# Kernel optimization log

Measured on AMD Instinct MI355X. Metric: run time of the kernel, lower is better.

Reference implementation:

```python
import jax, jax.numpy as jnp
import numpy as np

EPS = 1e-8

def _qparams(x, bits):
    # AsymmetricSignedQParams + GlobalMinMaxObserver: per-tensor min/max,
    # signed range [-2^(b-1), 2^(b-1)-1], asymmetric zero point.
    qmin = -(2 ** (bits - 1))
    qmax = 2 ** (bits - 1) - 1
    mn = jnp.minimum(jnp.min(x), 0.0)
    mx = jnp.maximum(jnp.max(x), 0.0)
    scale = jnp.maximum((mx - mn) / (qmax - qmin), EPS)
    zp = jnp.clip(jnp.round(qmin - mn / scale), qmin, qmax)
    return scale, zp, qmin, qmax

def _fake_quant(x, bits):
    # quantize -> clamp -> dequantize (simulated fixed-point as in float forward)
    scale, zp, qmin, qmax = _qparams(x, bits)
    q = jnp.clip(jnp.round(x / scale) + zp, qmin, qmax)
    return (q - zp) * scale


def setup_inputs() -> dict:
    key = jax.random.key(0)
    k1, k2, k3 = jax.random.split(key, 3)
    B, W, H, D = 8, 1024, 8, 64
    q = jax.random.normal(k1, (B, W, H, D), dtype=jnp.float32)
    k = jax.random.normal(k2, (B, W, H, D), dtype=jnp.float32)
    v = jax.random.normal(k3, (B, W, H, D), dtype=jnp.float32)
    return {"q": q, "k": k, "v": v, "quant_bits": 8}


def reference(q, k, v, quant_bits):
    bits = int(quant_bits)
    d_model = q.shape[-1]
    inv_sqrt_d = 1.0 / np.sqrt(d_model)

    # quantize-dequantize inputs (inputs_{q,k,v}_QParams)
    qf = _fake_quant(q, bits)
    kf = _fake_quant(k, bits)
    vf = _fake_quant(v, bits)

    # matrix_multi_score: quantized QK^T with folded 1/sqrt(d) scale,
    # then requantize output (matrix_multi_score.outputs_QParams)
    scores = jnp.einsum("bqhd,bkhd->bhqk", qf, kf) * inv_sqrt_d
    scores = _fake_quant(scores, bits)

    # SoftmaxLUT: softmax over last dim, result requantized (softmax.outputs_QParams)
    att = jax.nn.softmax(scores, axis=-1)
    att_q = _fake_quant(att, bits)

    # matrix_multi_att: quantized att @ V, requantized output
    context = jnp.einsum("bhqk,bkhd->bqhd", att_q, vf)
    context = _fake_quant(context, bits)

    return context, att_q
```

## Files before the change

kernel.cpp:

```cpp
#include <hip/hip_runtime.h>
#include <cstdint>
#include <cstddef>

#define W  1024
#define NH 8
#define NB 8
#define DH 64
#define BHN (NB*NH)
#define CTX_ELEMS ((size_t)NB*W*NH*DH)
#define NS 64
#define ROWF 512
#define L2E 1.4426950408889634f

typedef int v4i __attribute__((ext_vector_type(4)));


__device__ __forceinline__ unsigned enc_f(float f){
  unsigned u = __float_as_uint(f);
  return (u & 0x80000000u) ? ~u : (u | 0x80000000u);
}
__device__ __forceinline__ float dec_f(unsigned k){
  unsigned u = (k & 0x80000000u) ? (k ^ 0x80000000u) : ~k;
  return __uint_as_float(u);
}

__device__ __forceinline__ float fq1(float x, float s, float z, float mn, float mx){
  float t = rintf(x / s) + z;
  t = fminf(fmaxf(t, mn), mx);
  return (t - z) * s;
}
__device__ __forceinline__ int qint_m(float x, float is, float z, float mn, float mx){
  return (int)fminf(fmaxf(rintf(x * is) + z, mn), mx);
}
__device__ __forceinline__ unsigned pack4(int a0, int a1, int a2, int a3){
  return (unsigned)(a0 & 0xff) | ((unsigned)(a1 & 0xff) << 8) |
         ((unsigned)(a2 & 0xff) << 16) | ((unsigned)(a3 & 0xff) << 24);
}

__device__ __forceinline__ unsigned* slot_min(unsigned* s, int t){ return s + (size_t)(2*t)*NS; }
__device__ __forceinline__ unsigned* slot_max(unsigned* s, int t){ return s + (size_t)(2*t+1)*NS; }

struct QP { float s, z; };

__device__ __forceinline__ QP qp_generic(const unsigned* slots, int t, float qmn, float qmx){
  const unsigned* pm = slots + (size_t)(2*t)*NS;
  const unsigned* px = pm + NS;
  unsigned em = pm[0], ex = px[0];
  for (int i = 1; i < NS; ++i){
    unsigned a = pm[i], b = px[i];
    em = (a < em) ? a : em;
    ex = (b > ex) ? b : ex;
  }
  float mn = dec_f(em), mx = dec_f(ex);
  QP r;
  r.s = fmaxf((mx - mn) / (qmx - qmn), 1e-8f);
  r.z = fminf(fmaxf(rintf(qmn - mn / r.s), qmn), qmx);
  return r;
}
__device__ __forceinline__ QP qp_scores(const int* jmn, const int* jmx, float sq, float sk,
                                        float qmn, float qmx){
  int em = jmn[0], ex = jmx[0];
  for (int i = 1; i < NS; ++i){ em = min(em, jmn[i]); ex = max(ex, jmx[i]); }
  float cfac = 0.125f * (sq * sk);
  float mn = fminf(cfac * (float)em, 0.0f);
  float mx = fmaxf(cfac * (float)ex, 0.0f);
  QP r;
  r.s = fmaxf((mx - mn) / (qmx - qmn), 1e-8f);
  r.z = fminf(fmaxf(rintf(qmn - mn / r.s), qmn), qmx);
  return r;
}

__device__ __forceinline__ void blk_minmax_atomic(float lmin, float lmax,
                                                  unsigned* smin, unsigned* smax){
  #pragma unroll
  for (int o = 32; o; o >>= 1){
    lmin = fminf(lmin, __shfl_xor(lmin, o));
    lmax = fmaxf(lmax, __shfl_xor(lmax, o));
  }
  __shared__ float wmn[4], wmx[4];
  int wid = threadIdx.x >> 6, lane = threadIdx.x & 63;
  if (lane == 0){ wmn[wid] = lmin; wmx[wid] = lmax; }
  __syncthreads();
  if (threadIdx.x == 0){
    float a = wmn[0], b = wmx[0];
    for (int w = 1; w < (int)(blockDim.x >> 6); ++w){
      a = fminf(a, wmn[w]); b = fmaxf(b, wmx[w]);
    }
    atomicMin(smin, enc_f(a));
    atomicMax(smax, enc_f(b));
  }
}

__device__ __forceinline__ void blk_iminmax_atomic(int lmin, int lmax, int* gmin, int* gmax){
  #pragma unroll
  for (int o = 32; o; o >>= 1){
    lmin = min(lmin, __shfl_xor(lmin, o));
    lmax = max(lmax, __shfl_xor(lmax, o));
  }
  __shared__ int iwmn[4], iwmx[4];
  int wid = threadIdx.x >> 6, lane = threadIdx.x & 63;
  if (lane == 0){ iwmn[wid] = lmin; iwmx[wid] = lmax; }
  __syncthreads();
  if (threadIdx.x == 0){
    int a = iwmn[0], b = iwmx[0];
    for (int w = 1; w < (int)(blockDim.x >> 6); ++w){
      a = min(a, iwmn[w]); b = max(b, iwmx[w]);
    }
    atomicMin(gmin, a);
    atomicMax(gmax, b);
  }
}

__device__ __forceinline__ void stage_tile(const float* __restrict__ rowptr,
                                           signed char (*S)[80], int* __restrict__ Ssum,
                                           float is, float z, float mn, float mx, int t){
  const int rr = t >> 2, dq = (t & 3) << 4;
  const float* p = rowptr + (size_t)rr * ROWF + dq;
  int part = 0;
  #pragma unroll
  for (int g = 0; g < 4; ++g){
    float4 x = *(const float4*)(p + g * 4);
    int a0 = qint_m(x.x, is, z, mn, mx), a1 = qint_m(x.y, is, z, mn, mx);
    int a2 = qint_m(x.z, is, z, mn, mx), a3 = qint_m(x.w, is, z, mn, mx);
    part += a0 + a1 + a2 + a3;
    *(unsigned*)&S[rr][dq + g*4] = pack4(a0, a1, a2, a3);
  }
  int x1 = part + __shfl_xor(part, 1);
  int tot = x1 + __shfl_xor(x1, 2);
  if ((t & 3) == 0) Ssum[rr] = tot;
}

__device__ __forceinline__ v4i qfrag_direct(const float* __restrict__ qrow, int lg,
                                            float is, float z, float mn, float mx,
                                            int* sqi_out){
  const float* p = qrow + (lg << 4);
  int part = 0; unsigned d4[4];
  #pragma unroll
  for (int g = 0; g < 4; ++g){
    float4 x = *(const float4*)(p + g * 4);
    int a0 = qint_m(x.x, is, z, mn, mx), a1 = qint_m(x.y, is, z, mn, mx);
    int a2 = qint_m(x.z, is, z, mn, mx), a3 = qint_m(x.w, is, z, mn, mx);
    part += a0 + a1 + a2 + a3;
    d4[g] = pack4(a0, a1, a2, a3);
  }
  part += __shfl_xor(part, 16);
  part += __shfl_xor(part, 32);
  *sqi_out = part;
  v4i r; r[0] = (int)d4[0]; r[1] = (int)d4[1]; r[2] = (int)d4[2]; r[3] = (int)d4[3];
  return r;
}


__global__ void init_slots_kernel(unsigned* __restrict__ slots, int* __restrict__ jmn,
                                  int* __restrict__ jmx, int* __restrict__ Sv8){
  for (int i = threadIdx.x; i < 6*2*NS; i += blockDim.x)
    slots[i] = 0x80000000u;
  if (threadIdx.x < NS){
    jmn[threadIdx.x] = 0x7fffffff;
    jmx[threadIdx.x] = (int)0x80000000;
  }
  for (int i = threadIdx.x; i < BHN*64; i += blockDim.x) Sv8[i] = 0;
}

__global__ __launch_bounds__(256) void minmax3_kernel(const float* __restrict__ q,
                                                      const float* __restrict__ k,
                                                      const float* __restrict__ v,
                                                      unsigned* __restrict__ slots){
  const float4* p = (const float4*)(blockIdx.y == 0 ? q : (blockIdx.y == 1 ? k : v));
  float lmin = 0.f, lmax = 0.f;
  const int n4 = (int)(CTX_ELEMS / 4);
  for (int i = blockIdx.x * blockDim.x + threadIdx.x; i < n4; i += gridDim.x * blockDim.x){
    float4 x = p[i];
    lmin = fminf(lmin, fminf(fminf(x.x, x.y), fminf(x.z, x.w)));
    lmax = fmaxf(lmax, fmaxf(fmaxf(x.x, x.y), fmaxf(x.z, x.w)));
  }
  const int idx = blockIdx.x & (NS - 1);
  blk_minmax_atomic(lmin, lmax, slot_min(slots, blockIdx.y) + idx, slot_max(slots, blockIdx.y) + idx);
}


__global__ __launch_bounds__(256) void pass1a_kernel(const float* __restrict__ kg,
                                                     const float* __restrict__ vg,
                                                     const unsigned* __restrict__ slots,
                                                     const int* __restrict__ bits_p,
                                                     char* __restrict__ k8,
                                                     int* __restrict__ Sk8,
                                                     char* __restrict__ v8,
                                                     int* __restrict__ Sv8){
  __shared__ int ColS[64];
  const int bits = *bits_p;
  const float qmx = (float)((1 << (bits-1)) - 1), qmn = -(float)(1 << (bits-1));
  const QP kp = qp_generic(slots, 1, qmn, qmx);
  const QP vp = qp_generic(slots, 2, qmn, qmx);
  const int it = blockIdx.x, bh = blockIdx.y, b = bh >> 3, h = bh & 7;
  const int i0 = it << 6, t = threadIdx.x;

  {
    const int rr = t >> 2, dq = (t & 3) << 4;
    const float* p = kg + ((size_t)(b*W + i0 + rr) * NH + h) * DH + dq;
    const float isk = 1.0f / kp.s;
    int part = 0; unsigned d4[4];
    #pragma unroll
    for (int g = 0; g < 4; ++g){
      float4 x = *(const float4*)(p + g * 4);
      int a0 = qint_m(x.x, isk, kp.z, qmn, qmx), a1 = qint_m(x.y, isk, kp.z, qmn, qmx);
      int a2 = qint_m(x.z, isk, kp.z, qmn, qmx), a3 = qint_m(x.w, isk, kp.z, qmn, qmx);
      part += a0 + a1 + a2 + a3;
      d4[g] = pack4(a0, a1, a2, a3);
    }
    uint4 u; u.x = d4[0]; u.y = d4[1]; u.z = d4[2]; u.w = d4[3];
    *(uint4*)(k8 + ((size_t)bh << 16) + (((size_t)(i0 + rr)) << 6) + dq) = u;
    int x1 = part + __shfl_xor(part, 1);
    int tot = x1 + __shfl_xor(x1, 2);
    if ((t & 3) == 0) Sk8[(bh << 10) + i0 + rr] = tot;
  }

  {
    const int dq4 = (t & 15) << 2, kb = (t >> 4) << 2;
    const float* vp_ = vg + ((size_t)(b*W + i0 + kb) * NH + h) * DH + dq4;
    const float isv = 1.0f / vp.s;
    float4 x0 = *(const float4*)(vp_);
    float4 x1 = *(const float4*)(vp_ + ROWF);
    float4 x2 = *(const float4*)(vp_ + 2 * ROWF);
    float4 x3 = *(const float4*)(vp_ + 3 * ROWF);
    int q00 = qint_m(x0.x, isv, vp.z, qmn, qmx), q01 = qint_m(x0.y, isv, vp.z, qmn, qmx),
        q02 = qint_m(x0.z, isv, vp.z, qmn, qmx), q03 = qint_m(x0.w, isv, vp.z, qmn, qmx);
    int q10 = qint_m(x1.x, isv, vp.z, qmn, qmx), q11 = qint_m(x1.y, isv, vp.z, qmn, qmx),
        q12 = qint_m(x1.z, isv, vp.z, qmn, qmx), q13 = qint_m(x1.w, isv, vp.z, qmn, qmx);
    int q20 = qint_m(x2.x, isv, vp.z, qmn, qmx), q21 = qint_m(x2.y, isv, vp.z, qmn, qmx),
        q22 = qint_m(x2.z, isv, vp.z, qmn, qmx), q23 = qint_m(x2.w, isv, vp.z, qmn, qmx);
    int q30 = qint_m(x3.x, isv, vp.z, qmn, qmx), q31 = qint_m(x3.y, isv, vp.z, qmn, qmx),
        q32 = qint_m(x3.z, isv, vp.z, qmn, qmx), q33 = qint_m(x3.w, isv, vp.z, qmn, qmx);
    unsigned w0 = pack4(q00, q10, q20, q30);
    unsigned w1 = pack4(q01, q11, q21, q31);
    unsigned w2 = pack4(q02, q12, q22, q32);
    unsigned w3 = pack4(q03, q13, q23, q33);
    char* vb = v8 + ((size_t)bh << 16) + i0 + kb;
    *(unsigned*)(vb + ((size_t)(dq4 + 0) << 10)) = w0;
    *(unsigned*)(vb + ((size_t)(dq4 + 1) << 10)) = w1;
    *(unsigned*)(vb + ((size_t)(dq4 + 2) << 10)) = w2;
    *(unsigned*)(vb + ((size_t)(dq4 + 3) << 10)) = w3;
    int cv0 = q00 + q10 + q20 + q30;
    int cv1 = q01 + q11 + q21 + q31;
    int cv2 = q02 + q12 + q22 + q32;
    int cv3 = q03 + q13 + q23 + q33;
    if (t < 64) ColS[t] = 0;
    __syncthreads();
    atomicAdd(&ColS[dq4 + 0], cv0);
    atomicAdd(&ColS[dq4 + 1], cv1);
    atomicAdd(&ColS[dq4 + 2], cv2);
    atomicAdd(&ColS[dq4 + 3], cv3);
    __syncthreads();
    if (t < 64) atomicAdd(&Sv8[(bh << 6) + t], ColS[t]);
  }
}

__global__ __launch_bounds__(256) void pass1b_kernel(const float* __restrict__ qg,
                                                     const unsigned* __restrict__ slots,
                                                     const int* __restrict__ bits_p,
                                                     float* __restrict__ stash,
                                                     int* __restrict__ jmn,
                                                     int* __restrict__ jmx,
                                                     const char* __restrict__ k8,
                                                     const int* __restrict__ Sk8){
  const int bits = *bits_p;
  const float qmx = (float)((1 << (bits-1)) - 1), qmn = -(float)(1 << (bits-1));
  const QP qq = qp_generic(slots, 0, qmn, qmx);
  const QP kp = qp_generic(slots, 1, qmn, qmx);
  const int it = blockIdx.x, bh = blockIdx.y, b = bh >> 3, h = bh & 7;
  const int i0 = it << 6, t = threadIdx.x;
  const int lane = t & 63, w = t >> 6, lr = lane & 15, lg = lane >> 4;
  const int irow = (w << 4) + lr;
  const int izq = (int)qq.z, izk = (int)kp.z, c64 = 64 * izq * izk;

  int sqi;
  v4i Bq = qfrag_direct(qg + ((size_t)(b*W + i0 + irow) * NH + h) * DH, lg,
                        1.0f / qq.s, qq.z, qmn, qmx, &sqi);
  const char* kb = k8 + ((size_t)bh << 16);
  const int* skb = Sk8 + (bh << 10);

  int gmin = 0x7fffffff, gmax = (int)0x80000000, rmax = (int)0x80000000;
  for (int cc = 0; cc < 16; ++cc){
    #pragma unroll
    for (int jt = 0; jt < 4; ++jt){
      v4i Ak = *(const v4i*)(kb + (((size_t)((cc << 6) + (jt << 4) + lr)) << 6) + (lg << 4));
      v4i s4 = *(const v4i*)(skb + (cc << 6) + (jt << 4) + (lg << 2));
      v4i zz = {0, 0, 0, 0};
      v4i acc = __builtin_amdgcn_mfma_i32_16x16x64_i8(Ak, Bq, zz, 0, 0, 0);
      #pragma unroll
      for (int r = 0; r < 4; ++r){
        int J = acc[r] - izq * s4[r] - izk * sqi + c64;
        gmin = min(gmin, J); gmax = max(gmax, J); rmax = max(rmax, J);
      }
    }
  }
  rmax = max(rmax, __shfl_xor(rmax, 16));
  rmax = max(rmax, __shfl_xor(rmax, 32));
  if (lg == 0)
    stash[((size_t)(b*W + i0 + irow) * NH + h) * DH] = __int_as_float(rmax);
  const int idx = (it + bh * 16) & (NS - 1);
  blk_iminmax_atomic(gmin, gmax, jmn + idx, jmx + idx);
}

__global__ __launch_bounds__(256) void pass2c_kernel(const float* __restrict__ qg,
                                                     unsigned* __restrict__ slots,
                                                     const int* __restrict__ jmn,
                                                     const int* __restrict__ jmx,
                                                     const int* __restrict__ bits_p,
                                                     float* __restrict__ stash,
                                                     const char* __restrict__ k8,
                                                     const int* __restrict__ Sk8){
  const int bits = *bits_p;
  const float qmx = (float)((1 << (bits-1)) - 1), qmn = -(float)(1 << (bits-1));
  const QP qq = qp_generic(slots, 0, qmn, qmx);
  const QP kp = qp_generic(slots, 1, qmn, qmx);
  const QP sp = qp_scores(jmn, jmx, qq.s, kp.s, qmn, qmx);
  const int it = blockIdx.x, bh = blockIdx.y, b = bh >> 3, h = bh & 7;
  const int i0 = it << 6, t = threadIdx.x;
  const int lane = t & 63, w = t >> 6, lr = lane & 15, lg = lane >> 4;
  const int irow = (w << 4) + lr;
  const int izq = (int)qq.z, izk = (int)kp.z, c64 = 64 * izq * izk;
  const float rf = (0.125f * (qq.s * kp.s)) / sp.s;
  const float c2 = sp.s * L2E, zs = sp.z;

  int sqi;
  v4i Bq = qfrag_direct(qg + ((size_t)(b*W + i0 + irow) * NH + h) * DH, lg,
                        1.0f / qq.s, qq.z, qmn, qmx, &sqi);
  int Jm = __float_as_int(stash[((size_t)(b*W + i0 + irow) * NH + h) * DH]);
  const float tmxf = fminf(fmaxf(rintf((float)Jm * rf) + zs, qmn), qmx);
  const char* kb = k8 + ((size_t)bh << 16);
  const int* skb = Sk8 + (bh << 10);

  float zacc = 0.f;
  for (int cc = 0; cc < 16; ++cc){
    #pragma unroll
    for (int jt = 0; jt < 4; ++jt){
      v4i Ak = *(const v4i*)(kb + (((size_t)((cc << 6) + (jt << 4) + lr)) << 6) + (lg << 4));
      v4i s4 = *(const v4i*)(skb + (cc << 6) + (jt << 4) + (lg << 2));
      v4i zz = {0, 0, 0, 0};
      v4i acc = __builtin_amdgcn_mfma_i32_16x16x64_i8(Ak, Bq, zz, 0, 0, 0);
      int J0 = acc[0] - izq * s4[0] - izk * sqi + c64;
      int J1 = acc[1] - izq * s4[1] - izk * sqi + c64;
      int J2 = acc[2] - izq * s4[2] - izk * sqi + c64;
      int J3 = acc[3] - izq * s4[3] - izk * sqi + c64;
      float tl0 = fminf(fmaxf(rintf((float)J0 * rf) + zs, qmn), qmx);
      float tl1 = fminf(fmaxf(rintf((float)J1 * rf) + zs, qmn), qmx);
      float tl2 = fminf(fmaxf(rintf((float)J2 * rf) + zs, qmn), qmx);
      float tl3 = fminf(fmaxf(rintf((float)J3 * rf) + zs, qmn), qmx);
      zacc += exp2f((tl0 - tmxf) * c2);
      zacc += exp2f((tl1 - tmxf) * c2);
      zacc += exp2f((tl2 - tmxf) * c2);
      zacc += exp2f((tl3 - tmxf) * c2);
    }
  }
  zacc += __shfl_xor(zacc, 16);
  zacc += __shfl_xor(zacc, 32);
  if (lg == 0)
    stash[((size_t)(b*W + i0 + irow) * NH + h) * DH + 1] = zacc;
  float ratt = 1.0f / zacc;
  #pragma unroll
  for (int o = 1; o < 16; o <<= 1) ratt = fmaxf(ratt, __shfl_xor(ratt, o));
  if (lane == 0){
    const int idx = ((it << 2) + w + bh * 64) & (NS - 1);
    atomicMax(slot_max(slots, 4) + idx, enc_f(ratt));
  }
}

__global__ __launch_bounds__(256) void pass3c_kernel(const float* __restrict__ qg,
                                                     float* __restrict__ att,
                                                     float* __restrict__ ctx,
                                                     unsigned* __restrict__ slots,
                                                     const int* __restrict__ jmn,
                                                     const int* __restrict__ jmx,
                                                     const int* __restrict__ bits_p,
                                                     const char* __restrict__ k8,
                                                     const int* __restrict__ Sk8,
                                                     const char* __restrict__ v8,
                                                     const int* __restrict__ Sv8){
  __shared__ __align__(16) signed char As[64][80];
  __shared__ int RowA[64];
  const int bits = *bits_p;
  const float qmx = (float)((1 << (bits-1)) - 1), qmn = -(float)(1 << (bits-1));
  const QP qq = qp_generic(slots, 0, qmn, qmx);
  const QP kp = qp_generic(slots, 1, qmn, qmx);
  const QP sp = qp_scores(jmn, jmx, qq.s, kp.s, qmn, qmx);
  const QP vp = qp_generic(slots, 2, qmn, qmx);
  const QP ap = qp_generic(slots, 4, qmn, qmx);
  const int it = blockIdx.x, bh = blockIdx.y, b = bh >> 3, h = bh & 7;
  const int i0 = it << 6, t = threadIdx.x;
  const int lane = t & 63, w = t >> 6, lr = lane & 15, lg = lane >> 4;
  const int irow = (w << 4) + lr;
  const int izq = (int)qq.z, izk = (int)kp.z, c64 = 64 * izq * izk;
  const int iza = (int)ap.z, izv = (int)vp.z;
  const float rf = (0.125f * (qq.s * kp.s)) / sp.s;
  const float c2 = sp.s * L2E, zs = sp.z;
  const float sa = ap.s, za = ap.z, inv_sa = 1.0f / sa;

  int sqi;
  v4i Bq = qfrag_direct(qg + ((size_t)(b*W + i0 + irow) * NH + h) * DH, lg,
                        1.0f / qq.s, qq.z, qmn, qmx, &sqi);
  const size_t rbase = ((size_t)(b*W + i0 + irow) * NH + h) * DH;
  int Jm = __float_as_int(ctx[rbase]);
  const float tmxf = fminf(fmaxf(rintf((float)Jm * rf) + zs, qmn), qmx);
  const float iZ = 1.0f / ctx[rbase + 1];
  const char* kb = k8 + ((size_t)bh << 16);
  const int* skb = Sk8 + (bh << 10);
  const char* vb = v8 + ((size_t)bh << 16);

  int rA = 0;
  v4i accPV[4];
  #pragma unroll
  for (int tj = 0; tj < 4; ++tj){ v4i zz = {0,0,0,0}; accPV[tj] = zz; }

  for (int cc = 0; cc < 16; ++cc){
    #pragma unroll
    for (int jt = 0; jt < 4; ++jt){
      v4i Ak = *(const v4i*)(kb + (((size_t)((cc << 6) + (jt << 4) + lr)) << 6) + (lg << 4));
      v4i s4 = *(const v4i*)(skb + (cc << 6) + (jt << 4) + (lg << 2));
      v4i zz = {0, 0, 0, 0};
      v4i acc = __builtin_amdgcn_mfma_i32_16x16x64_i8(Ak, Bq, zz, 0, 0, 0);
      int J0 = acc[0] - izq * s4[0] - izk * sqi + c64;
      int J1 = acc[1] - izq * s4[1] - izk * sqi + c64;
      int J2 = acc[2] - izq * s4[2] - izk * sqi + c64;
      int J3 = acc[3] - izq * s4[3] - izk * sqi + c64;
      float tl0 = fminf(fmaxf(rintf((float)J0 * rf) + zs, qmn), qmx);
      float tl1 = fminf(fmaxf(rintf((float)J1 * rf) + zs, qmn), qmx);
      float tl2 = fminf(fmaxf(rintf((float)J2 * rf) + zs, qmn), qmx);
      float tl3 = fminf(fmaxf(rintf((float)J3 * rf) + zs, qmn), qmx);
      float p0 = exp2f((tl0 - tmxf) * c2) * iZ;
      float p1 = exp2f((tl1 - tmxf) * c2) * iZ;
      float p2 = exp2f((tl2 - tmxf) * c2) * iZ;
      float p3 = exp2f((tl3 - tmxf) * c2) * iZ;
      float a0 = fminf(fmaxf(rintf(p0 * inv_sa) + za, qmn), qmx);
      float a1 = fminf(fmaxf(rintf(p1 * inv_sa) + za, qmn), qmx);
      float a2 = fminf(fmaxf(rintf(p2 * inv_sa) + za, qmn), qmx);
      float a3 = fminf(fmaxf(rintf(p3 * inv_sa) + za, qmn), qmx);
      float4 y;
      y.x = (a0 - za) * sa; y.y = (a1 - za) * sa;
      y.z = (a2 - za) * sa; y.w = (a3 - za) * sa;
      *(float4*)(att + ((size_t)bh << 20) + (size_t)(i0 + irow) * W
                 + (cc << 6) + (jt << 4) + (lg << 2)) = y;
      int q0 = (int)a0, q1 = (int)a1, q2 = (int)a2, q3 = (int)a3;
      rA += q0 + q1 + q2 + q3;
      *(unsigned*)&As[irow][(jt << 4) + (lg << 2)] = pack4(q0, q1, q2, q3);
    }
    {
      v4i A2 = *(const v4i*)&As[(w << 4) + lr][lg << 4];
      #pragma unroll
      for (int tj = 0; tj < 4; ++tj){
        v4i B2 = *(const v4i*)(vb + (((size_t)((tj << 4) + lr)) << 10) + (cc << 6) + (lg << 4));
        accPV[tj] = __builtin_amdgcn_mfma_i32_16x16x64_i8(A2, B2, accPV[tj], 0, 0, 0);
      }
    }
  }

  rA += __shfl_xor(rA, 16);
  rA += __shfl_xor(rA, 32);
  if (lg == 0) RowA[irow] = rA;

  const float sav = sa * vp.s;
  float lmin = 0.f, lmax = 0.f;
  #pragma unroll
  for (int tj = 0; tj < 4; ++tj){
    const int d = (tj << 4) + lr;
    const int cvd = Sv8[(bh << 6) + d];
    #pragma unroll
    for (int r = 0; r < 4; ++r){
      const int i = (w << 4) + (lg << 2) + r;
      int Jv = accPV[tj][r] - iza * cvd - izv * RowA[i] + 1024 * iza * izv;
      float c = sav * (float)Jv;
      lmin = fminf(lmin, c); lmax = fmaxf(lmax, c);
      ctx[(((size_t)(b * W + i0 + i)) * NH + h) * DH + d] = c;
    }
  }
  const int idx = (it + bh * 16) & (NS - 1);
  blk_minmax_atomic(lmin, lmax, slot_min(slots, 5) + idx, slot_max(slots, 5) + idx);
}


__global__ __launch_bounds__(256) void pass1_plain(const float* __restrict__ qg,
                                                   const float* __restrict__ kg,
                                                   const unsigned* __restrict__ slots,
                                                   const int* __restrict__ bits_p,
                                                   float* __restrict__ stash,
                                                   int* __restrict__ jmn,
                                                   int* __restrict__ jmx){
  __shared__ __align__(16) signed char Qs[64][80], Ks[64][80];
  __shared__ int Sq[64], Sk[64];
  const int bits = *bits_p;
  const float qmx = (float)((1 << (bits-1)) - 1), qmn = -(float)(1 << (bits-1));
  const QP qq = qp_generic(slots, 0, qmn, qmx);
  const QP kp = qp_generic(slots, 1, qmn, qmx);
  const int it = blockIdx.x, bh = blockIdx.y, b = bh >> 3, h = bh & 7;
  const int i0 = it << 6, t = threadIdx.x;
  const int lane = t & 63, w = t >> 6, lr = lane & 15, lg = lane >> 4;
  const float isq = 1.0f / qq.s, isk = 1.0f / kp.s;
  const int izq = (int)qq.z, izk = (int)kp.z, c64 = 64 * izq * izk;

  stage_tile(qg + ((size_t)(b*W + i0) * NH + h) * DH, Qs, Sq, isq, qq.z, qmn, qmx, t);
  __syncthreads();
  const v4i Bq = *(const v4i*)&Qs[(w << 4) + lr][lg << 4];
  const int sqi = Sq[(w << 4) + lr];

  int gmin = 0x7fffffff, gmax = (int)0x80000000, rmax = (int)0x80000000;
  for (int cc = 0; cc < 16; ++cc){
    __syncthreads();
    stage_tile(kg + ((size_t)(b*W + (cc << 6)) * NH + h) * DH, Ks, Sk, isk, kp.z, qmn, qmx, t);
    __syncthreads();
    #pragma unroll
    for (int jt = 0; jt < 4; ++jt){
      v4i Ak = *(const v4i*)&Ks[(jt << 4) + lr][lg << 4];
      v4i zz = {0, 0, 0, 0};
      v4i acc = __builtin_amdgcn_mfma_i32_16x16x64_i8(Ak, Bq, zz, 0, 0, 0);
      v4i s4 = *(const v4i*)&Sk[(jt << 4) + (lg << 2)];
      #pragma unroll
      for (int r = 0; r < 4; ++r){
        int J = acc[r] - izq * s4[r] - izk * sqi + c64;
        gmin = min(gmin, J); gmax = max(gmax, J); rmax = max(rmax, J);
      }
    }
  }
  rmax = max(rmax, __shfl_xor(rmax, 16));
  rmax = max(rmax, __shfl_xor(rmax, 32));
  if (lg == 0)
    stash[((size_t)(b*W + i0 + (w << 4) + lr) * NH + h) * DH] = __int_as_float(rmax);
  const int idx = (it + bh * 16) & (NS - 1);
  blk_iminmax_atomic(gmin, gmax, jmn + idx, jmx + idx);
}

__global__ __launch_bounds__(256) void pass2_plain(const float* __restrict__ qg,
                                                   const float* __restrict__ kg,
                                                   unsigned* __restrict__ slots,
                                                   const int* __restrict__ jmn,
                                                   const int* __restrict__ jmx,
                                                   const int* __restrict__ bits_p,
                                                   float* __restrict__ stash){
  __shared__ __align__(16) signed char Qs[64][80], Ks[64][80];
  __shared__ int Sq[64], Sk[64];
  const int bits = *bits_p;
  const float qmx = (float)((1 << (bits-1)) - 1), qmn = -(float)(1 << (bits-1));
  const QP qq = qp_generic(slots, 0, qmn, qmx);
  const QP kp = qp_generic(slots, 1, qmn, qmx);
  const QP sp = qp_scores(jmn, jmx, qq.s, kp.s, qmn, qmx);
  const int it = blockIdx.x, bh = blockIdx.y, b = bh >> 3, h = bh & 7;
  const int i0 = it << 6, t = threadIdx.x;
  const int lane = t & 63, w = t >> 6, lr = lane & 15, lg = lane >> 4;
  const float isq = 1.0f / qq.s, isk = 1.0f / kp.s;
  const int izq = (int)qq.z, izk = (int)kp.z, c64 = 64 * izq * izk;
  const float rf = (0.125f * (qq.s * kp.s)) / sp.s;
  const float c2 = sp.s * L2E, zs = sp.z;
  const int irow = (w << 4) + lr;

  stage_tile(qg + ((size_t)(b*W + i0) * NH + h) * DH, Qs, Sq, isq, qq.z, qmn, qmx, t);
  __syncthreads();
  const v4i Bq = *(const v4i*)&Qs[irow][lg << 4];
  const int sqi = Sq[irow];
  int Jm = __float_as_int(stash[((size_t)(b*W + i0 + irow) * NH + h) * DH]);
  const float tmxf = fminf(fmaxf(rintf((float)Jm * rf) + zs, qmn), qmx);

  float zacc = 0.f;
  for (int cc = 0; cc < 16; ++cc){
    __syncthreads();
    stage_tile(kg + ((size_t)(b*W + (cc << 6)) * NH + h) * DH, Ks, Sk, isk, kp.z, qmn, qmx, t);
    __syncthreads();
    #pragma unroll
    for (int jt = 0; jt < 4; ++jt){
      v4i Ak = *(const v4i*)&Ks[(jt << 4) + lr][lg << 4];
      v4i zz = {0, 0, 0, 0};
      v4i acc = __builtin_amdgcn_mfma_i32_16x16x64_i8(Ak, Bq, zz, 0, 0, 0);
      v4i s4 = *(const v4i*)&Sk[(jt << 4) + (lg << 2)];
      int J0 = acc[0] - izq * s4[0] - izk * sqi + c64;
      int J1 = acc[1] - izq * s4[1] - izk * sqi + c64;
      int J2 = acc[2] - izq * s4[2] - izk * sqi + c64;
      int J3 = acc[3] - izq * s4[3] - izk * sqi + c64;
      float tl0 = fminf(fmaxf(rintf((float)J0 * rf) + zs, qmn), qmx);
      float tl1 = fminf(fmaxf(rintf((float)J1 * rf) + zs, qmn), qmx);
      float tl2 = fminf(fmaxf(rintf((float)J2 * rf) + zs, qmn), qmx);
      float tl3 = fminf(fmaxf(rintf((float)J3 * rf) + zs, qmn), qmx);
      zacc += exp2f((tl0 - tmxf) * c2);
      zacc += exp2f((tl1 - tmxf) * c2);
      zacc += exp2f((tl2 - tmxf) * c2);
      zacc += exp2f((tl3 - tmxf) * c2);
    }
  }
  zacc += __shfl_xor(zacc, 16);
  zacc += __shfl_xor(zacc, 32);
  if (lg == 0)
    stash[((size_t)(b*W + i0 + irow) * NH + h) * DH + 1] = zacc;
  float ratt = 1.0f / zacc;
  #pragma unroll
  for (int o = 1; o < 16; o <<= 1) ratt = fmaxf(ratt, __shfl_xor(ratt, o));
  if (lane == 0){
    const int idx = ((it << 2) + w + bh * 64) & (NS - 1);
    atomicMax(slot_max(slots, 4) + idx, enc_f(ratt));
  }
}

__global__ __launch_bounds__(256) void pass3_plain(const float* __restrict__ qg,
                                                   const float* __restrict__ kg,
                                                   const float* __restrict__ vg,
                                                   float* __restrict__ att,
                                                   float* __restrict__ ctx,
                                                   unsigned* __restrict__ slots,
                                                   const int* __restrict__ jmn,
                                                   const int* __restrict__ jmx,
                                                   const int* __restrict__ bits_p){
  __shared__ __align__(16) signed char Qs[64][80], Ks[64][80], Vs[64][80], As[64][80];
  __shared__ int Sq[64], Sk[64];
  __shared__ int RowA[64], ColV[64];
  const int bits = *bits_p;
  const float qmx = (float)((1 << (bits-1)) - 1), qmn = -(float)(1 << (bits-1));
  const QP qq = qp_generic(slots, 0, qmn, qmx);
  const QP kp = qp_generic(slots, 1, qmn, qmx);
  const QP sp = qp_scores(jmn, jmx, qq.s, kp.s, qmn, qmx);
  const QP vp = qp_generic(slots, 2, qmn, qmx);
  const QP ap = qp_generic(slots, 4, qmn, qmx);
  const int it = blockIdx.x, bh = blockIdx.y, b = bh >> 3, h = bh & 7;
  const int i0 = it << 6, t = threadIdx.x;
  const int lane = t & 63, w = t >> 6, lr = lane & 15, lg = lane >> 4;
  const float isq = 1.0f / qq.s, isk = 1.0f / kp.s;
  const int izq = (int)qq.z, izk = (int)kp.z, c64 = 64 * izq * izk;
  const float rf = (0.125f * (qq.s * kp.s)) / sp.s;
  const float c2 = sp.s * L2E, zs = sp.z;
  const float sa = ap.s, za = ap.z, inv_sa = 1.0f / sa;
  const float sv = vp.s, zv = vp.z, isv = 1.0f / sv;
  const int iza = (int)za, izv = (int)zv;
  const int irow = (w << 4) + lr;

  if (t < 64) ColV[t] = 0;
  stage_tile(qg + ((size_t)(b*W + i0) * NH + h) * DH, Qs, Sq, isq, qq.z, qmn, qmx, t);
  __syncthreads();
  const v4i Bq = *(const v4i*)&Qs[irow][lg << 4];
  const int sqi = Sq[irow];
  const size_t rbase = ((size_t)(b*W + i0 + irow) * NH + h) * DH;
  int Jm = __float_as_int(ctx[rbase]);
  const float tmxf = fminf(fmaxf(rintf((float)Jm * rf) + zs, qmn), qmx);
  const float iZ = 1.0f / ctx[rbase + 1];

  const int dq4 = (t & 15) << 2;
  const int kb  = (t >> 4) << 2;
  int cv4[4] = {0, 0, 0, 0};
  int rA = 0;
  v4i accPV[4];
  #pragma unroll
  for (int tj = 0; tj < 4; ++tj){ v4i zz = {0,0,0,0}; accPV[tj] = zz; }

  for (int cc = 0; cc < 16; ++cc){
    __syncthreads();
    stage_tile(kg + ((size_t)(b*W + (cc << 6)) * NH + h) * DH, Ks, Sk, isk, kp.z, qmn, qmx, t);
    {
      const float* vp_ = vg + ((size_t)(b*W + (cc << 6) + kb) * NH + h) * DH + dq4;
      float4 x0 = *(const float4*)(vp_);
      float4 x1 = *(const float4*)(vp_ + ROWF);
      float4 x2 = *(const float4*)(vp_ + 2 * ROWF);
      float4 x3 = *(const float4*)(vp_ + 3 * ROWF);
      int q00 = qint_m(x0.x, isv, zv, qmn, qmx), q01 = qint_m(x0.y, isv, zv, qmn, qmx),
          q02 = qint_m(x0.z, isv, zv, qmn, qmx), q03 = qint_m(x0.w, isv, zv, qmn, qmx);
      int q10 = qint_m(x1.x, isv, zv, qmn, qmx), q11 = qint_m(x1.y, isv, zv, qmn, qmx),
          q12 = qint_m(x1.z, isv, zv, qmn, qmx), q13 = qint_m(x1.w, isv, zv, qmn, qmx);
      int q20 = qint_m(x2.x, isv, zv, qmn, qmx), q21 = qint_m(x2.y, isv, zv, qmn, qmx),
          q22 = qint_m(x2.z, isv, zv, qmn, qmx), q23 = qint_m(x2.w, isv, zv, qmn, qmx);
      int q30 = qint_m(x3.x, isv, zv, qmn, qmx), q31 = qint_m(x3.y, isv, zv, qmn, qmx),
          q32 = qint_m(x3.z, isv, zv, qmn, qmx), q33 = qint_m(x3.w, isv, zv, qmn, qmx);
      cv4[0] += q00 + q10 + q20 + q30;
      cv4[1] += q01 + q11 + q21 + q31;
      cv4[2] += q02 + q12 + q22 + q32;
      cv4[3] += q03 + q13 + q23 + q33;
      *(unsigned*)&Vs[dq4 + 0][kb] = pack4(q00, q10, q20, q30);
      *(unsigned*)&Vs[dq4 + 1][kb] = pack4(q01, q11, q21, q31);
      *(unsigned*)&Vs[dq4 + 2][kb] = pack4(q02, q12, q22, q32);
      *(unsigned*)&Vs[dq4 + 3][kb] = pack4(q03, q13, q23, q33);
    }
    __syncthreads();
    #pragma unroll
    for (int jt = 0; jt < 4; ++jt){
      v4i Ak = *(const v4i*)&Ks[(jt << 4) + lr][lg << 4];
      v4i zz = {0, 0, 0, 0};
      v4i acc = __builtin_amdgcn_mfma_i32_16x16x64_i8(Ak, Bq, zz, 0, 0, 0);
      v4i s4 = *(const v4i*)&Sk[(jt << 4) + (lg << 2)];
      int J0 = acc[0] - izq * s4[0] - izk * sqi + c64;
      int J1 = acc[1] - izq * s4[1] - izk * sqi + c64;
      int J2 = acc[2] - izq * s4[2] - izk * sqi + c64;
      int J3 = acc[3] - izq * s4[3] - izk * sqi + c64;
      float tl0 = fminf(fmaxf(rintf((float)J0 * rf) + zs, qmn), qmx);
      float tl1 = fminf(fmaxf(rintf((float)J1 * rf) + zs, qmn), qmx);
      float tl2 = fminf(fmaxf(rintf((float)J2 * rf) + zs, qmn), qmx);
      float tl3 = fminf(fmaxf(rintf((float)J3 * rf) + zs, qmn), qmx);
      float p0 = exp2f((tl0 - tmxf) * c2) * iZ;
      float p1 = exp2f((tl1 - tmxf) * c2) * iZ;
      float p2 = exp2f((tl2 - tmxf) * c2) * iZ;
      float p3 = exp2f((tl3 - tmxf) * c2) * iZ;
      float a0 = fminf(fmaxf(rintf(p0 * inv_sa) + za, qmn), qmx);
      float a1 = fminf(fmaxf(rintf(p1 * inv_sa) + za, qmn), qmx);
      float a2 = fminf(fmaxf(rintf(p2 * inv_sa) + za, qmn), qmx);
      float a3 = fminf(fmaxf(rintf(p3 * inv_sa) + za, qmn), qmx);
      float4 y;
      y.x = (a0 - za) * sa; y.y = (a1 - za) * sa;
      y.z = (a2 - za) * sa; y.w = (a3 - za) * sa;
      *(float4*)(att + ((size_t)bh << 20) + (size_t)(i0 + irow) * W
                 + (cc << 6) + (jt << 4) + (lg << 2)) = y;
      int q0 = (int)a0, q1 = (int)a1, q2 = (int)a2, q3 = (int)a3;
      rA += q0 + q1 + q2 + q3;
      *(unsigned*)&As[irow][(jt << 4) + (lg << 2)] = pack4(q0, q1, q2, q3);
    }
    {
      v4i A2 = *(const v4i*)&As[(w << 4) + lr][lg << 4];
      #pragma unroll
      for (int tj = 0; tj < 4; ++tj){
        v4i B2 = *(const v4i*)&Vs[(tj << 4) + lr][lg << 4];
        accPV[tj] = __builtin_amdgcn_mfma_i32_16x16x64_i8(A2, B2, accPV[tj], 0, 0, 0);
      }
    }
  }

  rA += __shfl_xor(rA, 16);
  rA += __shfl_xor(rA, 32);
  if (lg == 0) RowA[irow] = rA;
  #pragma unroll
  for (int j = 0; j < 4; ++j) atomicAdd(&ColV[dq4 + j], cv4[j]);
  __syncthreads();

  const float sav = sa * sv;
  float lmin = 0.f, lmax = 0.f;
  #pragma unroll
  for (int tj = 0; tj < 4; ++tj){
    const int d = (tj << 4) + lr;
    #pragma unroll
    for (int r = 0; r < 4; ++r){
      const int i = (w << 4) + (lg << 2) + r;
      int Jv = accPV[tj][r] - iza * ColV[d] - izv * RowA[i] + 1024 * iza * izv;
      float c = sav * (float)Jv;
      lmin = fminf(lmin, c); lmax = fmaxf(lmax, c);
      ctx[(((size_t)(b * W + i0 + i)) * NH + h) * DH + d] = c;
    }
  }
  const int idx = (it + bh * 16) & (NS - 1);
  blk_minmax_atomic(lmin, lmax, slot_min(slots, 5) + idx, slot_max(slots, 5) + idx);
}

__global__ __launch_bounds__(256) void quantctx_kernel(float* __restrict__ ctx,
                                                       const unsigned* __restrict__ slots,
                                                       const int* __restrict__ bits_p){
  const int bits = *bits_p;
  const float qmx = (float)((1 << (bits-1)) - 1), qmn = -(float)(1 << (bits-1));
  const QP cp = qp_generic(slots, 5, qmn, qmx);
  size_t i = (size_t)blockIdx.x * blockDim.x + threadIdx.x;
  float4* p = (float4*)ctx;
  float4 x = p[i];
  x.x = fq1(x.x, cp.s, cp.z, qmn, qmx);
  x.y = fq1(x.y, cp.s, cp.z, qmn, qmx);
  x.z = fq1(x.z, cp.s, cp.z, qmn, qmx);
  x.w = fq1(x.w, cp.s, cp.z, qmn, qmx);
  p[i] = x;
}


extern "C" void kernel_launch(void* const* d_in, const int* in_sizes, int n_in,
                              void* d_out, int out_size, void* d_ws, size_t ws_size,
                              hipStream_t stream){
  const float* q = (const float*)d_in[0];
  const float* k = (const float*)d_in[1];
  const float* v = (const float*)d_in[2];
  const int* bits = (const int*)d_in[3];
  float* ctx = (float*)d_out;
  float* att = (float*)d_out + CTX_ELEMS;
  unsigned* slots = (unsigned*)d_ws;
  int* jmn = (int*)((char*)d_ws + 3072);
  int* jmx = (int*)((char*)d_ws + 3328);
  int* Sv8 = (int*)((char*)d_ws + 4096);
  int* Sk8 = (int*)((char*)d_ws + 20480);
  char* k8 = (char*)d_ws + 282624;
  char* v8 = (char*)d_ws + 4476928;
  const bool cached = ws_size >= (size_t)8671232;

  hipLaunchKernelGGL(init_slots_kernel, dim3(1), dim3(256), 0, stream, slots, jmn, jmx, Sv8);
  hipLaunchKernelGGL(minmax3_kernel, dim3(512, 3), dim3(256), 0, stream, q, k, v, slots);
  if (cached){
    hipLaunchKernelGGL(pass1a_kernel, dim3(16, BHN), dim3(256), 0, stream,
                       k, v, slots, bits, k8, Sk8, v8, Sv8);
    hipLaunchKernelGGL(pass1b_kernel, dim3(16, BHN), dim3(256), 0, stream,
                       q, slots, bits, ctx, jmn, jmx, k8, Sk8);
    hipLaunchKernelGGL(pass2c_kernel, dim3(16, BHN), dim3(256), 0, stream,
                       q, slots, jmn, jmx, bits, ctx, k8, Sk8);
    hipLaunchKernelGGL(pass3c_kernel, dim3(16, BHN), dim3(256), 0, stream,
                       q, att, ctx, slots, jmn, jmx, bits, k8, Sk8, v8, Sv8);
  } else {
    hipLaunchKernelGGL(pass1_plain, dim3(16, BHN), dim3(256), 0, stream,
                       q, k, slots, bits, ctx, jmn, jmx);
    hipLaunchKernelGGL(pass2_plain, dim3(16, BHN), dim3(256), 0, stream,
                       q, k, slots, jmn, jmx, bits, ctx);
    hipLaunchKernelGGL(pass3_plain, dim3(16, BHN), dim3(256), 0, stream,
                       q, k, v, att, ctx, slots, jmn, jmx, bits);
  }
  hipLaunchKernelGGL(quantctx_kernel, dim3(4096), dim3(256), 0, stream, ctx, slots, bits);
}
```

Measured before the change: 210.5 us.

## Cache int8-quantized Q once and reuse across passes; nontemporal att stores

Adds a workspace tier that quantizes Q to int8 with row sums once in pass1a, so pass1b, pass2c and pass3c load packed int8 fragments instead of re-reading and re-quantizing fp32 Q three times. The V fragments for the PV MFMA are now loaded at the top of each chunk loop so their latency can overlap with the QK and softmax work. The attention output is written with nontemporal stores to avoid polluting cache. The Q-cache path only runs when the workspace is large enough, and it adds extra writes in pass1a.

```diff
diff --git a/kernel.cpp b/kernel.cpp
--- a/kernel.cpp
+++ b/kernel.cpp
@@ -13,6 +13,7 @@
 #define L2E 1.4426950408889634f
 
 typedef int v4i __attribute__((ext_vector_type(4)));
+typedef float v4f __attribute__((ext_vector_type(4)));
 
 
 __device__ __forceinline__ unsigned enc_f(float f){
@@ -178,15 +179,18 @@
   blk_minmax_atomic(lmin, lmax, slot_min(slots, blockIdx.y) + idx, slot_max(slots, blockIdx.y) + idx);
 }
 
-
-__global__ __launch_bounds__(256) void pass1a_kernel(const float* __restrict__ kg,
+template<bool QC>
+__global__ __launch_bounds__(256) void pass1a_kernel(const float* __restrict__ qg,
+                                                     const float* __restrict__ kg,
                                                      const float* __restrict__ vg,
                                                      const unsigned* __restrict__ slots,
                                                      const int* __restrict__ bits_p,
                                                      char* __restrict__ k8,
                                                      int* __restrict__ Sk8,
                                                      char* __restrict__ v8,
-                                                     int* __restrict__ Sv8){
+                                                     int* __restrict__ Sv8,
+                                                     char* __restrict__ q8,
+                                                     int* __restrict__ Sq8){
   __shared__ int ColS[64];
   const int bits = *bits_p;
   const float qmx = (float)((1 << (bits-1)) - 1), qmn = -(float)(1 << (bits-1));
@@ -194,9 +198,9 @@
   const QP vp = qp_generic(slots, 2, qmn, qmx);
   const int it = blockIdx.x, bh = blockIdx.y, b = bh >> 3, h = bh & 7;
   const int i0 = it << 6, t = threadIdx.x;
+  const int rr = t >> 2, dq = (t & 3) << 4;
 
   {
-    const int rr = t >> 2, dq = (t & 3) << 4;
     const float* p = kg + ((size_t)(b*W + i0 + rr) * NH + h) * DH + dq;
     const float isk = 1.0f / kp.s;
     int part = 0; unsigned d4[4];
@@ -214,7 +218,25 @@
     int tot = x1 + __shfl_xor(x1, 2);
     if ((t & 3) == 0) Sk8[(bh << 10) + i0 + rr] = tot;
   }
-
+  if (QC){
+    const QP qq = qp_generic(slots, 0, qmn, qmx);
+    const float* p = qg + ((size_t)(b*W + i0 + rr) * NH + h) * DH + dq;
+    const float isq = 1.0f / qq.s;
+    int part = 0; unsigned d4[4];
+    #pragma unroll
+    for (int g = 0; g < 4; ++g){
+      float4 x = *(const float4*)(p + g * 4);
+      int a0 = qint_m(x.x, isq, qq.z, qmn, qmx), a1 = qint_m(x.y, isq, qq.z, qmn, qmx);
+      int a2 = qint_m(x.z, isq, qq.z, qmn, qmx), a3 = qint_m(x.w, isq, qq.z, qmn, qmx);
+      part += a0 + a1 + a2 + a3;
+      d4[g] = pack4(a0, a1, a2, a3);
+    }
+    uint4 u; u.x = d4[0]; u.y = d4[1]; u.z = d4[2]; u.w = d4[3];
+    *(uint4*)(q8 + ((size_t)bh << 16) + (((size_t)(i0 + rr)) << 6) + dq) = u;
+    int x1 = part + __shfl_xor(part, 1);
+    int tot = x1 + __shfl_xor(x1, 2);
+    if ((t & 3) == 0) Sq8[(bh << 10) + i0 + rr] = tot;
+  }
   {
     const int dq4 = (t & 15) << 2, kb = (t >> 4) << 2;
     const float* vp_ = vg + ((size_t)(b*W + i0 + kb) * NH + h) * DH + dq4;
@@ -231,30 +253,38 @@
         q22 = qint_m(x2.z, isv, vp.z, qmn, qmx), q23 = qint_m(x2.w, isv, vp.z, qmn, qmx);
     int q30 = qint_m(x3.x, isv, vp.z, qmn, qmx), q31 = qint_m(x3.y, isv, vp.z, qmn, qmx),
         q32 = qint_m(x3.z, isv, vp.z, qmn, qmx), q33 = qint_m(x3.w, isv, vp.z, qmn, qmx);
-    unsigned w0 = pack4(q00, q10, q20, q30);
-    unsigned w1 = pack4(q01, q11, q21, q31);
-    unsigned w2 = pack4(q02, q12, q22, q32);
-    unsigned w3 = pack4(q03, q13, q23, q33);
     char* vb = v8 + ((size_t)bh << 16) + i0 + kb;
-    *(unsigned*)(vb + ((size_t)(dq4 + 0) << 10)) = w0;
-    *(unsigned*)(vb + ((size_t)(dq4 + 1) << 10)) = w1;
-    *(unsigned*)(vb + ((size_t)(dq4 + 2) << 10)) = w2;
-    *(unsigned*)(vb + ((size_t)(dq4 + 3) << 10)) = w3;
-    int cv0 = q00 + q10 + q20 + q30;
-    int cv1 = q01 + q11 + q21 + q31;
-    int cv2 = q02 + q12 + q22 + q32;
-    int cv3 = q03 + q13 + q23 + q33;
+    *(unsigned*)(vb + ((size_t)(dq4 + 0) << 10)) = pack4(q00, q10, q20, q30);
+    *(unsigned*)(vb + ((size_t)(dq4 + 1) << 10)) = pack4(q01, q11, q21, q31);
+    *(unsigned*)(vb + ((size_t)(dq4 + 2) << 10)) = pack4(q02, q12, q22, q32);
+    *(unsigned*)(vb + ((size_t)(dq4 + 3) << 10)) = pack4(q03, q13, q23, q33);
     if (t < 64) ColS[t] = 0;
     __syncthreads();
-    atomicAdd(&ColS[dq4 + 0], cv0);
-    atomicAdd(&ColS[dq4 + 1], cv1);
-    atomicAdd(&ColS[dq4 + 2], cv2);
-    atomicAdd(&ColS[dq4 + 3], cv3);
+    atomicAdd(&ColS[dq4 + 0], q00 + q10 + q20 + q30);
+    atomicAdd(&ColS[dq4 + 1], q01 + q11 + q21 + q31);
+    atomicAdd(&ColS[dq4 + 2], q02 + q12 + q22 + q32);
+    atomicAdd(&ColS[dq4 + 3], q03 + q13 + q23 + q33);
     __syncthreads();
     if (t < 64) atomicAdd(&Sv8[(bh << 6) + t], ColS[t]);
   }
 }
 
+template<bool QC>
+__device__ __forceinline__ v4i get_bq(const float* __restrict__ qg,
+                                      const char* __restrict__ q8,
+                                      const int* __restrict__ Sq8,
+                                      int b, int h, int bh, int i0, int irow, int lg,
+                                      float isq, float zq, float qmn, float qmx,
+                                      int* sqi_out){
+  if (QC){
+    *sqi_out = Sq8[(bh << 10) + i0 + irow];
+    return *(const v4i*)(q8 + ((size_t)bh << 16) + (((size_t)(i0 + irow)) << 6) + (lg << 4));
+  }
+  return qfrag_direct(qg + ((size_t)(b*W + i0 + irow) * NH + h) * DH, lg,
+                      isq, zq, qmn, qmx, sqi_out);
+}
+
+template<bool QC>
 __global__ __launch_bounds__(256) void pass1b_kernel(const float* __restrict__ qg,
                                                      const unsigned* __restrict__ slots,
                                                      const int* __restrict__ bits_p,
@@ -262,7 +292,9 @@
                                                      int* __restrict__ jmn,
                                                      int* __restrict__ jmx,
                                                      const char* __restrict__ k8,
-                                                     const int* __restrict__ Sk8){
+                                                     const int* __restrict__ Sk8,
+                                                     const char* __restrict__ q8,
+                                                     const int* __restrict__ Sq8){
   const int bits = *bits_p;
   const float qmx = (float)((1 << (bits-1)) - 1), qmn = -(float)(1 << (bits-1));
   const QP qq = qp_generic(slots, 0, qmn, qmx);
@@ -274,8 +306,7 @@
   const int izq = (int)qq.z, izk = (int)kp.z, c64 = 64 * izq * izk;
 
   int sqi;
-  v4i Bq = qfrag_direct(qg + ((size_t)(b*W + i0 + irow) * NH + h) * DH, lg,
-                        1.0f / qq.s, qq.z, qmn, qmx, &sqi);
+  v4i Bq = get_bq<QC>(qg, q8, Sq8, b, h, bh, i0, irow, lg, 1.0f / qq.s, qq.z, qmn, qmx, &sqi);
   const char* kb = k8 + ((size_t)bh << 16);
   const int* skb = Sk8 + (bh << 10);
 
@@ -302,6 +333,7 @@
   blk_iminmax_atomic(gmin, gmax, jmn + idx, jmx + idx);
 }
 
+template<bool QC>
 __global__ __launch_bounds__(256) void pass2c_kernel(const float* __restrict__ qg,
                                                      unsigned* __restrict__ slots,
                                                      const int* __restrict__ jmn,
@@ -309,7 +341,9 @@
                                                      const int* __restrict__ bits_p,
                                                      float* __restrict__ stash,
                                                      const char* __restrict__ k8,
-                                                     const int* __restrict__ Sk8){
+                                                     const int* __restrict__ Sk8,
+                                                     const char* __restrict__ q8,
+                                                     const int* __restrict__ Sq8){
   const int bits = *bits_p;
   const float qmx = (float)((1 << (bits-1)) - 1), qmn = -(float)(1 << (bits-1));
   const QP qq = qp_generic(slots, 0, qmn, qmx);
@@ -324,8 +358,7 @@
   const float c2 = sp.s * L2E, zs = sp.z;
 
   int sqi;
-  v4i Bq = qfrag_direct(qg + ((size_t)(b*W + i0 + irow) * NH + h) * DH, lg,
-                        1.0f / qq.s, qq.z, qmn, qmx, &sqi);
+  v4i Bq = get_bq<QC>(qg, q8, Sq8, b, h, bh, i0, irow, lg, 1.0f / qq.s, qq.z, qmn, qmx, &sqi);
   int Jm = __float_as_int(stash[((size_t)(b*W + i0 + irow) * NH + h) * DH]);
   const float tmxf = fminf(fmaxf(rintf((float)Jm * rf) + zs, qmn), qmx);
   const char* kb = k8 + ((size_t)bh << 16);
@@ -366,6 +399,7 @@
   }
 }
 
+template<bool QC>
 __global__ __launch_bounds__(256) void pass3c_kernel(const float* __restrict__ qg,
                                                      float* __restrict__ att,
                                                      float* __restrict__ ctx,
@@ -376,7 +410,9 @@
                                                      const char* __restrict__ k8,
                                                      const int* __restrict__ Sk8,
                                                      const char* __restrict__ v8,
-                                                     const int* __restrict__ Sv8){
+                                                     const int* __restrict__ Sv8,
+                                                     const char* __restrict__ q8,
+                                                     const int* __restrict__ Sq8){
   __shared__ __align__(16) signed char As[64][80];
   __shared__ int RowA[64];
   const int bits = *bits_p;
@@ -397,8 +433,7 @@
   const float sa = ap.s, za = ap.z, inv_sa = 1.0f / sa;
 
   int sqi;
-  v4i Bq = qfrag_direct(qg + ((size_t)(b*W + i0 + irow) * NH + h) * DH, lg,
-                        1.0f / qq.s, qq.z, qmn, qmx, &sqi);
+  v4i Bq = get_bq<QC>(qg, q8, Sq8, b, h, bh, i0, irow, lg, 1.0f / qq.s, qq.z, qmn, qmx, &sqi);
   const size_t rbase = ((size_t)(b*W + i0 + irow) * NH + h) * DH;
   int Jm = __float_as_int(ctx[rbase]);
   const float tmxf = fminf(fmaxf(rintf((float)Jm * rf) + zs, qmn), qmx);
@@ -413,6 +448,10 @@
   for (int tj = 0; tj < 4; ++tj){ v4i zz = {0,0,0,0}; accPV[tj] = zz; }
 
   for (int cc = 0; cc < 16; ++cc){
+    v4i Bv[4];
+    #pragma unroll
+    for (int tj = 0; tj < 4; ++tj)
+      Bv[tj] = *(const v4i*)(vb + (((size_t)((tj << 4) + lr)) << 10) + (cc << 6) + (lg << 4));
     #pragma unroll
     for (int jt = 0; jt < 4; ++jt){
       v4i Ak = *(const v4i*)(kb + (((size_t)((cc << 6) + (jt << 4) + lr)) << 6) + (lg << 4));
@@ -435,11 +474,11 @@
       float a1 = fminf(fmaxf(rintf(p1 * inv_sa) + za, qmn), qmx);
       float a2 = fminf(fmaxf(rintf(p2 * inv_sa) + za, qmn), qmx);
       float a3 = fminf(fmaxf(rintf(p3 * inv_sa) + za, qmn), qmx);
-      float4 y;
-      y.x = (a0 - za) * sa; y.y = (a1 - za) * sa;
-      y.z = (a2 - za) * sa; y.w = (a3 - za) * sa;
-      *(float4*)(att + ((size_t)bh << 20) + (size_t)(i0 + irow) * W
-                 + (cc << 6) + (jt << 4) + (lg << 2)) = y;
+      v4f y;
+      y[0] = (a0 - za) * sa; y[1] = (a1 - za) * sa;
+      y[2] = (a2 - za) * sa; y[3] = (a3 - za) * sa;
+      __builtin_nontemporal_store(y, (v4f*)(att + ((size_t)bh << 20)
+                 + (size_t)(i0 + irow) * W + (cc << 6) + (jt << 4) + (lg << 2)));
       int q0 = (int)a0, q1 = (int)a1, q2 = (int)a2, q3 = (int)a3;
       rA += q0 + q1 + q2 + q3;
       *(unsigned*)&As[irow][(jt << 4) + (lg << 2)] = pack4(q0, q1, q2, q3);
@@ -447,10 +486,8 @@
     {
       v4i A2 = *(const v4i*)&As[(w << 4) + lr][lg << 4];
       #pragma unroll
-      for (int tj = 0; tj < 4; ++tj){
-        v4i B2 = *(const v4i*)(vb + (((size_t)((tj << 4) + lr)) << 10) + (cc << 6) + (lg << 4));
-        accPV[tj] = __builtin_amdgcn_mfma_i32_16x16x64_i8(A2, B2, accPV[tj], 0, 0, 0);
-      }
+      for (int tj = 0; tj < 4; ++tj)
+        accPV[tj] = __builtin_amdgcn_mfma_i32_16x16x64_i8(A2, Bv[tj], accPV[tj], 0, 0, 0);
     }
   }
 
@@ -569,18 +606,12 @@
       v4i zz = {0, 0, 0, 0};
       v4i acc = __builtin_amdgcn_mfma_i32_16x16x64_i8(Ak, Bq, zz, 0, 0, 0);
       v4i s4 = *(const v4i*)&Sk[(jt << 4) + (lg << 2)];
-      int J0 = acc[0] - izq * s4[0] - izk * sqi + c64;
-      int J1 = acc[1] - izq * s4[1] - izk * sqi + c64;
-      int J2 = acc[2] - izq * s4[2] - izk * sqi + c64;
-      int J3 = acc[3] - izq * s4[3] - izk * sqi + c64;
-      float tl0 = fminf(fmaxf(rintf((float)J0 * rf) + zs, qmn), qmx);
-      float tl1 = fminf(fmaxf(rintf((float)J1 * rf) + zs, qmn), qmx);
-      float tl2 = fminf(fmaxf(rintf((float)J2 * rf) + zs, qmn), qmx);
-      float tl3 = fminf(fmaxf(rintf((float)J3 * rf) + zs, qmn), qmx);
-      zacc += exp2f((tl0 - tmxf) * c2);
-      zacc += exp2f((tl1 - tmxf) * c2);
-      zacc += exp2f((tl2 - tmxf) * c2);
-      zacc += exp2f((tl3 - tmxf) * c2);
+      #pragma unroll
+      for (int r = 0; r < 4; ++r){
+        int J = acc[r] - izq * s4[r] - izk * sqi + c64;
+        float tl = fminf(fmaxf(rintf((float)J * rf) + zs, qmn), qmx);
+        zacc += exp2f((tl - tmxf) * c2);
+      }
     }
   }
   zacc += __shfl_xor(zacc, 16);
@@ -771,19 +802,31 @@
   int* Sk8 = (int*)((char*)d_ws + 20480);
   char* k8 = (char*)d_ws + 282624;
   char* v8 = (char*)d_ws + 4476928;
-  const bool cached = ws_size >= (size_t)8671232;
+  int* Sq8 = (int*)((char*)d_ws + 8671232);
+  char* q8 = (char*)d_ws + 8933376;
+  const bool t1 = ws_size >= (size_t)8671232;
+  const bool t2 = ws_size >= (size_t)13127680;
 
   hipLaunchKernelGGL(init_slots_kernel, dim3(1), dim3(256), 0, stream, slots, jmn, jmx, Sv8);
   hipLaunchKernelGGL(minmax3_kernel, dim3(512, 3), dim3(256), 0, stream, q, k, v, slots);
-  if (cached){
-    hipLaunchKernelGGL(pass1a_kernel, dim3(16, BHN), dim3(256), 0, stream,
-                       k, v, slots, bits, k8, Sk8, v8, Sv8);
-    hipLaunchKernelGGL(pass1b_kernel, dim3(16, BHN), dim3(256), 0, stream,
-                       q, slots, bits, ctx, jmn, jmx, k8, Sk8);
-    hipLaunchKernelGGL(pass2c_kernel, dim3(16, BHN), dim3(256), 0, stream,
-                       q, slots, jmn, jmx, bits, ctx, k8, Sk8);
-    hipLaunchKernelGGL(pass3c_kernel, dim3(16, BHN), dim3(256), 0, stream,
-                       q, att, ctx, slots, jmn, jmx, bits, k8, Sk8, v8, Sv8);
+  if (t2){
+    hipLaunchKernelGGL(pass1a_kernel<true>, dim3(16, BHN), dim3(256), 0, stream,
+                       q, k, v, slots, bits, k8, Sk8, v8, Sv8, q8, Sq8);
+    hipLaunchKernelGGL(pass1b_kernel<true>, dim3(16, BHN), dim3(256), 0, stream,
+                       q, slots, bits, ctx, jmn, jmx, k8, Sk8, q8, Sq8);
+    hipLaunchKernelGGL(pass2c_kernel<true>, dim3(16, BHN), dim3(256), 0, stream,
+                       q, slots, jmn, jmx, bits, ctx, k8, Sk8, q8, Sq8);
+    hipLaunchKernelGGL(pass3c_kernel<true>, dim3(16, BHN), dim3(256), 0, stream,
+                       q, att, ctx, slots, jmn, jmx, bits, k8, Sk8, v8, Sv8, q8, Sq8);
+  } else if (t1){
+    hipLaunchKernelGGL(pass1a_kernel<false>, dim3(16, BHN), dim3(256), 0, stream,
+                       q, k, v, slots, bits, k8, Sk8, v8, Sv8, q8, Sq8);
+    hipLaunchKernelGGL(pass1b_kernel<false>, dim3(16, BHN), dim3(256), 0, stream,
+                       q, slots, bits, ctx, jmn, jmx, k8, Sk8, q8, Sq8);
+    hipLaunchKernelGGL(pass2c_kernel<false>, dim3(16, BHN), dim3(256), 0, stream,
+                       q, slots, jmn, jmx, bits, ctx, k8, Sk8, q8, Sq8);
+    hipLaunchKernelGGL(pass3c_kernel<false>, dim3(16, BHN), dim3(256), 0, stream,
+                       q, att, ctx, slots, jmn, jmx, bits, k8, Sk8, v8, Sv8, q8, Sq8);
   } else {
     hipLaunchKernelGGL(pass1_plain, dim3(16, BHN), dim3(256), 0, stream,
                        q, k, slots, bits, ctx, jmn, jmx);
```

New measurement: 235.4 us. +11.8%, slower.
